# Optimization experiments

Hardware: AMD Instinct MI355X
Metric: run time of the kernel (lower is better)

The kernel has to match this reference:

```python
import jax, jax.numpy as jnp
import numpy as np

N, K, C = 128, 64, 64

def _w(key, shape, scale):
    return (jax.random.normal(key, shape, dtype=jnp.float32) * scale)

def setup_inputs() -> dict:
    key = jax.random.key(0)
    ks = jax.random.split(key, 20)
    s1 = 1.0 / np.sqrt(C)
    s2 = 1.0 / np.sqrt(2 * C)
    inp = {
        "x": jax.random.normal(ks[0], (N, K, C), dtype=jnp.float32),
        "W_lin": _w(ks[1], (C, C), s1), "b_lin": jnp.zeros((C,), jnp.float32),
        # unary_passing: Linear(C,C) -> tanh -> Linear(C,C)
        "Wu1": _w(ks[2], (C, C), s1), "bu1": jnp.zeros((C,), jnp.float32),
        "Wu2": _w(ks[3], (C, C), s1), "bu2": jnp.zeros((C,), jnp.float32),
        # unary_gate: Linear(C,C) -> tanh -> Linear(C,C) -> sigmoid
        "Wug1": _w(ks[4], (C, C), s1), "bug1": jnp.zeros((C,), jnp.float32),
        "Wug2": _w(ks[5], (C, C), s1), "bug2": jnp.zeros((C,), jnp.float32),
        # binary_passing: Linear(2C,C) -> tanh -> Linear(C,C)
        "Wb1": _w(ks[6], (2 * C, C), s2), "bb1": jnp.zeros((C,), jnp.float32),
        "Wb2": _w(ks[7], (C, C), s1), "bb2": jnp.zeros((C,), jnp.float32),
        # binary_gate: Linear(2C,C) -> tanh -> Linear(C,C) -> sigmoid
        "Wbg1": _w(ks[8], (2 * C, C), s2), "bbg1": jnp.zeros((C,), jnp.float32),
        "Wbg2": _w(ks[9], (C, C), s1), "bbg2": jnp.zeros((C,), jnp.float32),
        "t": 0,  # time scalar, ignored by IgnoreLinear base layer
    }
    return inp


def reference(x, W_lin, b_lin, Wu1, bu1, Wu2, bu2, Wug1, bug1, Wug2, bug2,
              Wb1, bb1, Wb2, bb2, Wbg1, bbg1, Wbg2, bbg2, t):
    # base linear map (IgnoreLinear: ignores t)
    h = x @ W_lin + b_lin                          # (N, K, C)
    n, k, c = h.shape
    # unary message with gate
    um = jnp.tanh(h @ Wu1 + bu1) @ Wu2 + bu2
    ug = jax.nn.sigmoid(jnp.tanh(h @ Wug1 + bug1) @ Wug2 + bug2)
    um = um * ug                                   # (N, K, C)
    # all-pairs broadcast-concat: hm[n,i,j] = [h[n,j], h[n,i]]
    hm = jnp.concatenate([
        jnp.broadcast_to(h[:, None, :, :], (n, k, k, c)),
        jnp.broadcast_to(h[:, :, None, :], (n, k, k, c)),
    ], axis=3)                                     # (N, K, K, 2C)
    bm = jnp.tanh(hm @ Wb1 + bb1) @ Wb2 + bb2      # (N, K, K, C)
    bg = jax.nn.sigmoid(jnp.tanh(hm @ Wbg1 + bbg1) @ Wbg2 + bbg2)
    # sum over axis 1 (includes diagonal, as in original), normalize by K-1
    bm = jnp.sum(bm * bg, axis=1) / jnp.float32(k - 1)  # (N, K, C)
    return um + bm
```

## Files before the change

### kernel.cpp

```cpp
#include <hip/hip_runtime.h>

#define WST 72

typedef __attribute__((ext_vector_type(4))) float    f32x4;
typedef __attribute__((ext_vector_type(2))) float    f32x2;
typedef __attribute__((ext_vector_type(8))) _Float16 f16x8;
typedef __attribute__((ext_vector_type(2))) _Float16 f16x2;

__device__ __forceinline__ float rcp_f(float x) { return __builtin_amdgcn_rcpf(x); }
__device__ __forceinline__ float fast_sigmoid(float x) {
    return rcp_f(1.0f + __expf(-x));
}
__device__ __forceinline__ float tanh_exp(float x) {
    return 1.0f - 2.0f * rcp_f(__expf(2.0f * x) + 1.0f);
}

__device__ __forceinline__ void stage512(const float* __restrict__ W,
                                         _Float16* Wt, int tid) {
#pragma unroll
    for (int i = 0; i < 8; ++i) {
        int idx = tid + i * 512;
        int k = idx >> 6, c = idx & 63;
        Wt[c * WST + k] = (_Float16)W[idx];
    }
}

__device__ __forceinline__ void gemm2(const _Float16* Act, int arow, int qd,
                                      const _Float16* Wt, int colb,
                                      f32x4 acc[2]) {
    f16x8 a0 = *(const f16x8*)(Act + arow * WST + qd * 8);
    f16x8 a1 = *(const f16x8*)(Act + arow * WST + 32 + qd * 8);
#pragma unroll
    for (int cc = 0; cc < 2; ++cc) {
        const _Float16* wr = Wt + (colb + cc * 16) * WST + qd * 8;
        f16x8 b0 = *(const f16x8*)(wr);
        f16x8 b1 = *(const f16x8*)(wr + 32);
        acc[cc] = __builtin_amdgcn_mfma_f32_16x16x32_f16(a0, b0, acc[cc], 0, 0, 0);
        acc[cc] = __builtin_amdgcn_mfma_f32_16x16x32_f16(a1, b1, acc[cc], 0, 0, 0);
    }
}

__global__ __launch_bounds__(512, 2) void fused_all_kernel(
    const float* __restrict__ x,
    const float* __restrict__ W_lin, const float* __restrict__ b_lin,
    const float* __restrict__ Wu1,  const float* __restrict__ bu1,
    const float* __restrict__ Wu2,  const float* __restrict__ bu2,
    const float* __restrict__ Wug1, const float* __restrict__ bug1,
    const float* __restrict__ Wug2, const float* __restrict__ bug2,
    const float* __restrict__ Wb1,  const float* __restrict__ bb1,
    const float* __restrict__ Wb2,  const float* __restrict__ bb2,
    const float* __restrict__ Wbg1, const float* __restrict__ bbg1,
    const float* __restrict__ Wbg2, const float* __restrict__ bbg2,
    float* __restrict__ out)
{
    __shared__ __align__(16) char smem[113664];
    _Float16* Wt0  = (_Float16*)(smem);
    _Float16* Wt1  = (_Float16*)(smem + 9216);
    _Float16* Ax   = (_Float16*)(smem + 18432);
    _Float16* Ah   = (_Float16*)(smem + 27648);
    _Float16* Au   = (_Float16*)(smem + 36864);
    _Float16* Agg  = (_Float16*)(smem + 46080);
    float*    EQb  = (float*)(smem + 55296);
    float*    EQgb = (float*)(smem + 71680);
    float*    EPm  = (float*)(smem + 88064);
    float*    EPgm = (float*)(smem + 96768);
    float*    um32 = (float*)(smem + 105472);
    float*    Red  = (float*)(smem);

    int tid = threadIdx.x, w = tid >> 6, l = tid & 63;
    int qd = l >> 4, l16 = l & 15;
    int n = blockIdx.x >> 1, jsel = blockIdx.x & 1;

    int rw = w & 3, ch = w >> 2;
    int arow = rw * 16 + l16;
    int colb = ch * 32 + l16;
    int crow = rw * 16 + qd * 4;
    bool mine = (rw >> 1) == jsel;
    int lr0 = (rw & 1) * 16 + qd * 4;

    f32x4 acc[2];

#pragma unroll
    for (int i = 0; i < 4; ++i) {
        int e = tid * 2 + i * 1024;
        f32x2 v = *(const f32x2*)(x + (size_t)n * 4096 + e);
        f16x2 p; p[0] = (_Float16)v[0]; p[1] = (_Float16)v[1];
        *(f16x2*)(Ax + (e >> 6) * WST + (e & 63)) = p;
    }
    stage512(W_lin, Wt0, tid);
    __syncthreads();

#pragma unroll
    for (int cc = 0; cc < 2; ++cc) {
        float bv = b_lin[colb + cc * 16];
        acc[cc] = (f32x4){bv, bv, bv, bv};
    }
    gemm2(Ax, arow, qd, Wt0, colb, acc);
#pragma unroll
    for (int cc = 0; cc < 2; ++cc)
#pragma unroll
        for (int r = 0; r < 4; ++r)
            Ah[(crow + r) * WST + colb + cc * 16] = (_Float16)acc[cc][r];
    stage512(Wb1, Wt1, tid);
    __syncthreads();

#pragma unroll
    for (int cc = 0; cc < 2; ++cc) {
        float bv = bb1[colb + cc * 16];
        acc[cc] = (f32x4){bv, bv, bv, bv};
    }
    gemm2(Ah, arow, qd, Wt1, colb, acc);
    if (mine) {
#pragma unroll
        for (int cc = 0; cc < 2; ++cc)
#pragma unroll
            for (int r = 0; r < 4; ++r)
                EPm[(lr0 + r) * 68 + colb + cc * 16] = __expf(2.0f * acc[cc][r]);
    }
    stage512(Wb1 + 4096, Wt0, tid);
    __syncthreads();

    acc[0] = (f32x4){0.f, 0.f, 0.f, 0.f};
    acc[1] = (f32x4){0.f, 0.f, 0.f, 0.f};
    gemm2(Ah, arow, qd, Wt0, colb, acc);
#pragma unroll
    for (int cc = 0; cc < 2; ++cc)
#pragma unroll
        for (int r = 0; r < 4; ++r)
            EQb[(crow + r) * 64 + colb + cc * 16] = __expf(2.0f * acc[cc][r]);
    stage512(Wbg1, Wt1, tid);
    __syncthreads();

#pragma unroll
    for (int cc = 0; cc < 2; ++cc) {
        float bv = bbg1[colb + cc * 16];
        acc[cc] = (f32x4){bv, bv, bv, bv};
    }
    gemm2(Ah, arow, qd, Wt1, colb, acc);
    if (mine) {
#pragma unroll
        for (int cc = 0; cc < 2; ++cc)
#pragma unroll
            for (int r = 0; r < 4; ++r)
                EPgm[(lr0 + r) * 68 + colb + cc * 16] = __expf(2.0f * acc[cc][r]);
    }
    stage512(Wbg1 + 4096, Wt0, tid);
    __syncthreads();

    acc[0] = (f32x4){0.f, 0.f, 0.f, 0.f};
    acc[1] = (f32x4){0.f, 0.f, 0.f, 0.f};
    gemm2(Ah, arow, qd, Wt0, colb, acc);
#pragma unroll
    for (int cc = 0; cc < 2; ++cc)
#pragma unroll
        for (int r = 0; r < 4; ++r)
            EQgb[(crow + r) * 64 + colb + cc * 16] = __expf(2.0f * acc[cc][r]);
    stage512(Wu1, Wt1, tid);
    __syncthreads();

#pragma unroll
    for (int cc = 0; cc < 2; ++cc) {
        float bv = bu1[colb + cc * 16];
        acc[cc] = (f32x4){bv, bv, bv, bv};
    }
    gemm2(Ah, arow, qd, Wt1, colb, acc);
#pragma unroll
    for (int cc = 0; cc < 2; ++cc)
#pragma unroll
        for (int r = 0; r < 4; ++r)
            Au[(crow + r) * WST + colb + cc * 16] = (_Float16)tanh_exp(acc[cc][r]);
    stage512(Wug1, Wt0, tid);
    __syncthreads();

#pragma unroll
    for (int cc = 0; cc < 2; ++cc) {
        float bv = bug1[colb + cc * 16];
        acc[cc] = (f32x4){bv, bv, bv, bv};
    }
    gemm2(Ah, arow, qd, Wt0, colb, acc);
#pragma unroll
    for (int cc = 0; cc < 2; ++cc)
#pragma unroll
        for (int r = 0; r < 4; ++r)
            Agg[(crow + r) * WST + colb + cc * 16] = (_Float16)tanh_exp(acc[cc][r]);
    stage512(Wu2, Wt1, tid);
    __syncthreads();

    f32x4 uacc[2];
#pragma unroll
    for (int cc = 0; cc < 2; ++cc) {
        float bv = bu2[colb + cc * 16];
        uacc[cc] = (f32x4){bv, bv, bv, bv};
    }
    gemm2(Au, arow, qd, Wt1, colb, uacc);
    stage512(Wug2, Wt0, tid);
    __syncthreads();

#pragma unroll
    for (int cc = 0; cc < 2; ++cc) {
        float bv = bug2[colb + cc * 16];
        acc[cc] = (f32x4){bv, bv, bv, bv};
    }
    gemm2(Agg, arow, qd, Wt0, colb, acc);
    if (mine) {
#pragma unroll
        for (int cc = 0; cc < 2; ++cc)
#pragma unroll
            for (int r = 0; r < 4; ++r)
                um32[(lr0 + r) * 64 + colb + cc * 16] =
                    uacc[cc][r] * fast_sigmoid(acc[cc][r]);
    }
    stage512(Wb2, Wt1, tid);
    stage512(Wbg2, Au, tid);
    __syncthreads();

    int jgrp = w >> 2, iw = w & 3;

    f16x8 bwm[4][2], bwg[4][2];
#pragma unroll
    for (int cc = 0; cc < 4; ++cc)
#pragma unroll
        for (int kk = 0; kk < 2; ++kk) {
            bwm[cc][kk] = *(const f16x8*)(Wt1 + (cc * 16 + l16) * WST + kk * 32 + qd * 8);
            bwg[cc][kk] = *(const f16x8*)(Au  + (cc * 16 + l16) * WST + kk * 32 + qd * 8);
        }
    float bim[4], big[4];
#pragma unroll
    for (int cc = 0; cc < 4; ++cc) {
        bim[cc] = bb2[cc * 16 + l16];
        big[cc] = bbg2[cc * 16 + l16];
    }

    const float* pr  = EPm  + (jgrp * 16 + l16) * 68;
    const float* pgr = EPgm + (jgrp * 16 + l16) * 68;
    f32x4 pm[4], pg[4];
    pm[0] = *(const f32x4*)(pr + qd * 8);
    pm[1] = *(const f32x4*)(pr + qd * 8 + 4);
    pm[2] = *(const f32x4*)(pr + 32 + qd * 8);
    pm[3] = *(const f32x4*)(pr + 32 + qd * 8 + 4);
    pg[0] = *(const f32x4*)(pgr + qd * 8);
    pg[1] = *(const f32x4*)(pgr + qd * 8 + 4);
    pg[2] = *(const f32x4*)(pgr + 32 + qd * 8);
    pg[3] = *(const f32x4*)(pgr + 32 + qd * 8 + 4);

    f32x4 bacc[4];
#pragma unroll
    for (int cc = 0; cc < 4; ++cc) bacc[cc] = (f32x4){0.f, 0.f, 0.f, 0.f};

    for (int ii = iw * 16; ii < iw * 16 + 16; ++ii) {
        const float* qm = EQb  + ii * 64;
        const float* qg = EQgb + ii * 64;
        f16x8 am[2], ag[2];
#pragma unroll
        for (int kk = 0; kk < 2; ++kk) {
            int cb = kk * 32 + qd * 8;
            f32x4 qa = *(const f32x4*)(qm + cb);
            f32x4 qb = *(const f32x4*)(qm + cb + 4);
            f32x4 ha = *(const f32x4*)(qg + cb);
            f32x4 hb = *(const f32x4*)(qg + cb + 4);
#pragma unroll
            for (int t = 0; t < 4; ++t) {
                am[kk][t]     = (_Float16)(1.0f - 2.0f * rcp_f(__builtin_fmaf(pm[kk*2][t],   qa[t], 1.0f)));
                am[kk][t + 4] = (_Float16)(1.0f - 2.0f * rcp_f(__builtin_fmaf(pm[kk*2+1][t], qb[t], 1.0f)));
                ag[kk][t]     = (_Float16)(1.0f - 2.0f * rcp_f(__builtin_fmaf(pg[kk*2][t],   ha[t], 1.0f)));
                ag[kk][t + 4] = (_Float16)(1.0f - 2.0f * rcp_f(__builtin_fmaf(pg[kk*2+1][t], hb[t], 1.0f)));
            }
        }
#pragma unroll
        for (int cc = 0; cc < 4; ++cc) {
            f32x4 d = {bim[cc], bim[cc], bim[cc], bim[cc]};
            d = __builtin_amdgcn_mfma_f32_16x16x32_f16(am[0], bwm[cc][0], d, 0, 0, 0);
            d = __builtin_amdgcn_mfma_f32_16x16x32_f16(am[1], bwm[cc][1], d, 0, 0, 0);
            f32x4 e = {big[cc], big[cc], big[cc], big[cc]};
            e = __builtin_amdgcn_mfma_f32_16x16x32_f16(ag[0], bwg[cc][0], e, 0, 0, 0);
            e = __builtin_amdgcn_mfma_f32_16x16x32_f16(ag[1], bwg[cc][1], e, 0, 0, 0);
#pragma unroll
            for (int r = 0; r < 4; ++r)
                bacc[cc][r] += d[r] * fast_sigmoid(e[r]);
        }
    }

    __syncthreads();
#pragma unroll
    for (int cc = 0; cc < 4; ++cc)
#pragma unroll
        for (int r = 0; r < 4; ++r)
            Red[(jgrp * 4 + iw) * 1024 + (qd * 4 + r) * 64 + cc * 16 + l16] = bacc[cc][r];
    __syncthreads();

    {
        int e = tid * 4;
        int lr = e >> 6, col = e & 63;
        int g = lr >> 4, rr = lr & 15;
        f32x4 s = {0.f, 0.f, 0.f, 0.f};
#pragma unroll
        for (int w2 = 0; w2 < 4; ++w2)
            s += *(const f32x4*)(Red + (g * 4 + w2) * 1024 + rr * 64 + col);
        f32x4 u = *(const f32x4*)(um32 + lr * 64 + col);
        f32x4 o;
#pragma unroll
        for (int t = 0; t < 4; ++t)
            o[t] = u[t] + s[t] * (1.0f / 63.0f);
        *(f32x4*)(out + (size_t)n * 4096 + (size_t)(jsel * 32 + lr) * 64 + col) = o;
    }
}

extern "C" void kernel_launch(void* const* d_in, const int* in_sizes, int n_in,
                              void* d_out, int out_size, void* d_ws, size_t ws_size,
                              hipStream_t stream)
{
    (void)in_sizes; (void)n_in; (void)out_size; (void)d_ws; (void)ws_size;
    const float* x     = (const float*)d_in[0];
    const float* W_lin = (const float*)d_in[1];
    const float* b_lin = (const float*)d_in[2];
    const float* Wu1   = (const float*)d_in[3];
    const float* bu1   = (const float*)d_in[4];
    const float* Wu2   = (const float*)d_in[5];
    const float* bu2   = (const float*)d_in[6];
    const float* Wug1  = (const float*)d_in[7];
    const float* bug1  = (const float*)d_in[8];
    const float* Wug2  = (const float*)d_in[9];
    const float* bug2  = (const float*)d_in[10];
    const float* Wb1   = (const float*)d_in[11];
    const float* bb1   = (const float*)d_in[12];
    const float* Wb2   = (const float*)d_in[13];
    const float* bb2   = (const float*)d_in[14];
    const float* Wbg1  = (const float*)d_in[15];
    const float* bbg1  = (const float*)d_in[16];
    const float* Wbg2  = (const float*)d_in[17];
    const float* bbg2  = (const float*)d_in[18];

    hipLaunchKernelGGL(fused_all_kernel, dim3(256), dim3(512), 0, stream,
        x, W_lin, b_lin, Wu1, bu1, Wu2, bu2, Wug1, bug1, Wug2, bug2,
        Wb1, bb1, Wb2, bb2, Wbg1, bbg1, Wbg2, bbg2,
        (float*)d_out);
}
```

Baseline: 118.7 us.

## Double block size, restructure prologue staging, and fold tanh/sigmoid algebra into weights

Launches 1024-thread blocks instead of 512, splitting the prologue GEMMs so each wave computes one 16-column tile and restaging weights into registers ahead of use to overlap global loads with compute. The tanh affine part is folded into pre-scaled second-layer weights and column-sum biases, the sigmoid uses exp2 with a pre-multiplied log2e, and pairs of reciprocals share one rcp via a product trick with packed fp16 conversion. The main pair loop runs 8 rows per wave across 16 waves, and the reduction sums 8 partials. This trades the previous two-blocks-per-CU occupancy for one larger block, and the shared reciprocals risk overflow or precision loss.

Result: slower. 194.1 us (+63.6%).

```diff
diff --git a/kernel.cpp b/kernel.cpp
--- a/kernel.cpp
+++ b/kernel.cpp
@@ -1,46 +1,55 @@
 #include <hip/hip_runtime.h>
 
 #define WST 72
+#define LOG2E 1.44269504f
 
 typedef __attribute__((ext_vector_type(4))) float    f32x4;
 typedef __attribute__((ext_vector_type(2))) float    f32x2;
 typedef __attribute__((ext_vector_type(8))) _Float16 f16x8;
+typedef __attribute__((ext_vector_type(4))) _Float16 f16x4;
 typedef __attribute__((ext_vector_type(2))) _Float16 f16x2;
+typedef __attribute__((ext_vector_type(2))) __fp16   fp16x2_raw;
+
+union U8 { f16x8 v; f16x2 h[4]; };
 
 __device__ __forceinline__ float rcp_f(float x) { return __builtin_amdgcn_rcpf(x); }
+__device__ __forceinline__ float exp2_f(float x) { return __builtin_amdgcn_exp2f(x); }
 __device__ __forceinline__ float fast_sigmoid(float x) {
     return rcp_f(1.0f + __expf(-x));
 }
 __device__ __forceinline__ float tanh_exp(float x) {
     return 1.0f - 2.0f * rcp_f(__expf(2.0f * x) + 1.0f);
 }
-
-__device__ __forceinline__ void stage512(const float* __restrict__ W,
-                                         _Float16* Wt, int tid) {
-#pragma unroll
-    for (int i = 0; i < 8; ++i) {
-        int idx = tid + i * 512;
-        int k = idx >> 6, c = idx & 63;
-        Wt[c * WST + k] = (_Float16)W[idx];
-    }
-}
-
-__device__ __forceinline__ void gemm2(const _Float16* Act, int arow, int qd,
-                                      const _Float16* Wt, int colb,
-                                      f32x4 acc[2]) {
+__device__ __forceinline__ f16x2 pkrtz(float a, float b) {
+    fp16x2_raw r = __builtin_amdgcn_cvt_pkrtz(a, b);
+    return __builtin_bit_cast(f16x2, r);
+}
+
+__device__ __forceinline__ void wload4(const float* __restrict__ W, int tid, float v[4]) {
+#pragma unroll
+    for (int i = 0; i < 4; ++i) v[i] = W[tid + i * 1024];
+}
+__device__ __forceinline__ void wstore4(_Float16* Wt, int tid, const float v[4], float scale) {
+#pragma unroll
+    for (int i = 0; i < 4; ++i) {
+        int idx = tid + i * 1024;
+        Wt[(idx & 63) * WST + (idx >> 6)] = (_Float16)(v[i] * scale);
+    }
+}
+
+__device__ __forceinline__ f32x4 gemm1(const _Float16* Act, int arow, int qd,
+                                       const _Float16* Wt, int bcol, f32x4 acc) {
     f16x8 a0 = *(const f16x8*)(Act + arow * WST + qd * 8);
     f16x8 a1 = *(const f16x8*)(Act + arow * WST + 32 + qd * 8);
-#pragma unroll
-    for (int cc = 0; cc < 2; ++cc) {
-        const _Float16* wr = Wt + (colb + cc * 16) * WST + qd * 8;
-        f16x8 b0 = *(const f16x8*)(wr);
-        f16x8 b1 = *(const f16x8*)(wr + 32);
-        acc[cc] = __builtin_amdgcn_mfma_f32_16x16x32_f16(a0, b0, acc[cc], 0, 0, 0);
-        acc[cc] = __builtin_amdgcn_mfma_f32_16x16x32_f16(a1, b1, acc[cc], 0, 0, 0);
-    }
-}
-
-__global__ __launch_bounds__(512, 2) void fused_all_kernel(
+    const _Float16* wr = Wt + bcol * WST + qd * 8;
+    f16x8 b0 = *(const f16x8*)(wr);
+    f16x8 b1 = *(const f16x8*)(wr + 32);
+    acc = __builtin_amdgcn_mfma_f32_16x16x32_f16(a0, b0, acc, 0, 0, 0);
+    acc = __builtin_amdgcn_mfma_f32_16x16x32_f16(a1, b1, acc, 0, 0, 0);
+    return acc;
+}
+
+__global__ __launch_bounds__(1024) void fused_all_kernel(
     const float* __restrict__ x,
     const float* __restrict__ W_lin, const float* __restrict__ b_lin,
     const float* __restrict__ Wu1,  const float* __restrict__ bu1,
@@ -53,182 +62,181 @@
     const float* __restrict__ Wbg2, const float* __restrict__ bbg2,
     float* __restrict__ out)
 {
-    __shared__ __align__(16) char smem[113664];
-    _Float16* Wt0  = (_Float16*)(smem);
-    _Float16* Wt1  = (_Float16*)(smem + 9216);
-    _Float16* Ax   = (_Float16*)(smem + 18432);
-    _Float16* Ah   = (_Float16*)(smem + 27648);
-    _Float16* Au   = (_Float16*)(smem + 36864);
-    _Float16* Agg  = (_Float16*)(smem + 46080);
-    float*    EQb  = (float*)(smem + 55296);
-    float*    EQgb = (float*)(smem + 71680);
-    float*    EPm  = (float*)(smem + 88064);
-    float*    EPgm = (float*)(smem + 96768);
+    __shared__ __align__(16) char smem[114176];
+    _Float16* S0 = (_Float16*)(smem);
+    _Float16* S1 = (_Float16*)(smem + 9216);
+    _Float16* S2 = (_Float16*)(smem + 18432);
+    _Float16* S3 = (_Float16*)(smem + 27648);
+    _Float16* S4 = (_Float16*)(smem + 36864);
+    _Float16* S5 = (_Float16*)(smem + 46080);
+    float*    EPm  = (float*)(smem + 55296);
+    float*    EPgm = (float*)(smem + 64000);
+    float*    EQb  = (float*)(smem + 72704);
+    float*    EQgb = (float*)(smem + 89088);
     float*    um32 = (float*)(smem + 105472);
+    float*    csum_m = (float*)(smem + 113664);
+    float*    csum_g = (float*)(smem + 113920);
     float*    Red  = (float*)(smem);
 
     int tid = threadIdx.x, w = tid >> 6, l = tid & 63;
     int qd = l >> 4, l16 = l & 15;
     int n = blockIdx.x >> 1, jsel = blockIdx.x & 1;
 
-    int rw = w & 3, ch = w >> 2;
-    int arow = rw * 16 + l16;
-    int colb = ch * 32 + l16;
-    int crow = rw * 16 + qd * 4;
-    bool mine = (rw >> 1) == jsel;
-    int lr0 = (rw & 1) * 16 + qd * 4;
-
-    f32x4 acc[2];
-
-#pragma unroll
-    for (int i = 0; i < 4; ++i) {
-        int e = tid * 2 + i * 1024;
-        f32x2 v = *(const f32x2*)(x + (size_t)n * 4096 + e);
-        f16x2 p; p[0] = (_Float16)v[0]; p[1] = (_Float16)v[1];
-        *(f16x2*)(Ax + (e >> 6) * WST + (e & 63)) = p;
-    }
-    stage512(W_lin, Wt0, tid);
-    __syncthreads();
-
-#pragma unroll
-    for (int cc = 0; cc < 2; ++cc) {
-        float bv = b_lin[colb + cc * 16];
-        acc[cc] = (f32x4){bv, bv, bv, bv};
-    }
-    gemm2(Ax, arow, qd, Wt0, colb, acc);
-#pragma unroll
-    for (int cc = 0; cc < 2; ++cc)
-#pragma unroll
-        for (int r = 0; r < 4; ++r)
-            Ah[(crow + r) * WST + colb + cc * 16] = (_Float16)acc[cc][r];
-    stage512(Wb1, Wt1, tid);
-    __syncthreads();
-
-#pragma unroll
-    for (int cc = 0; cc < 2; ++cc) {
-        float bv = bb1[colb + cc * 16];
-        acc[cc] = (f32x4){bv, bv, bv, bv};
-    }
-    gemm2(Ah, arow, qd, Wt1, colb, acc);
-    if (mine) {
-#pragma unroll
-        for (int cc = 0; cc < 2; ++cc)
-#pragma unroll
-            for (int r = 0; r < 4; ++r)
-                EPm[(lr0 + r) * 68 + colb + cc * 16] = __expf(2.0f * acc[cc][r]);
-    }
-    stage512(Wb1 + 4096, Wt0, tid);
-    __syncthreads();
-
-    acc[0] = (f32x4){0.f, 0.f, 0.f, 0.f};
-    acc[1] = (f32x4){0.f, 0.f, 0.f, 0.f};
-    gemm2(Ah, arow, qd, Wt0, colb, acc);
-#pragma unroll
-    for (int cc = 0; cc < 2; ++cc)
-#pragma unroll
-        for (int r = 0; r < 4; ++r)
-            EQb[(crow + r) * 64 + colb + cc * 16] = __expf(2.0f * acc[cc][r]);
-    stage512(Wbg1, Wt1, tid);
-    __syncthreads();
-
-#pragma unroll
-    for (int cc = 0; cc < 2; ++cc) {
-        float bv = bbg1[colb + cc * 16];
-        acc[cc] = (f32x4){bv, bv, bv, bv};
-    }
-    gemm2(Ah, arow, qd, Wt1, colb, acc);
-    if (mine) {
-#pragma unroll
-        for (int cc = 0; cc < 2; ++cc)
-#pragma unroll
-            for (int r = 0; r < 4; ++r)
-                EPgm[(lr0 + r) * 68 + colb + cc * 16] = __expf(2.0f * acc[cc][r]);
-    }
-    stage512(Wbg1 + 4096, Wt0, tid);
-    __syncthreads();
-
-    acc[0] = (f32x4){0.f, 0.f, 0.f, 0.f};
-    acc[1] = (f32x4){0.f, 0.f, 0.f, 0.f};
-    gemm2(Ah, arow, qd, Wt0, colb, acc);
-#pragma unroll
-    for (int cc = 0; cc < 2; ++cc)
-#pragma unroll
-        for (int r = 0; r < 4; ++r)
-            EQgb[(crow + r) * 64 + colb + cc * 16] = __expf(2.0f * acc[cc][r]);
-    stage512(Wu1, Wt1, tid);
-    __syncthreads();
-
-#pragma unroll
-    for (int cc = 0; cc < 2; ++cc) {
-        float bv = bu1[colb + cc * 16];
-        acc[cc] = (f32x4){bv, bv, bv, bv};
-    }
-    gemm2(Ah, arow, qd, Wt1, colb, acc);
-#pragma unroll
-    for (int cc = 0; cc < 2; ++cc)
-#pragma unroll
-        for (int r = 0; r < 4; ++r)
-            Au[(crow + r) * WST + colb + cc * 16] = (_Float16)tanh_exp(acc[cc][r]);
-    stage512(Wug1, Wt0, tid);
-    __syncthreads();
-
-#pragma unroll
-    for (int cc = 0; cc < 2; ++cc) {
-        float bv = bug1[colb + cc * 16];
-        acc[cc] = (f32x4){bv, bv, bv, bv};
-    }
-    gemm2(Ah, arow, qd, Wt0, colb, acc);
-#pragma unroll
-    for (int cc = 0; cc < 2; ++cc)
-#pragma unroll
-        for (int r = 0; r < 4; ++r)
-            Agg[(crow + r) * WST + colb + cc * 16] = (_Float16)tanh_exp(acc[cc][r]);
-    stage512(Wu2, Wt1, tid);
-    __syncthreads();
-
-    f32x4 uacc[2];
-#pragma unroll
-    for (int cc = 0; cc < 2; ++cc) {
-        float bv = bu2[colb + cc * 16];
-        uacc[cc] = (f32x4){bv, bv, bv, bv};
-    }
-    gemm2(Au, arow, qd, Wt1, colb, uacc);
-    stage512(Wug2, Wt0, tid);
-    __syncthreads();
-
-#pragma unroll
-    for (int cc = 0; cc < 2; ++cc) {
-        float bv = bug2[colb + cc * 16];
-        acc[cc] = (f32x4){bv, bv, bv, bv};
-    }
-    gemm2(Agg, arow, qd, Wt0, colb, acc);
-    if (mine) {
-#pragma unroll
-        for (int cc = 0; cc < 2; ++cc)
-#pragma unroll
-            for (int r = 0; r < 4; ++r)
-                um32[(lr0 + r) * 64 + colb + cc * 16] =
-                    uacc[cc][r] * fast_sigmoid(acc[cc][r]);
-    }
-    stage512(Wb2, Wt1, tid);
-    stage512(Wbg2, Au, tid);
-    __syncthreads();
-
-    int jgrp = w >> 2, iw = w & 3;
+    int rw = w & 3, cw = w >> 2;
+    int arow64 = rw * 16 + l16;
+    int bcol64 = cw * 16 + l16;
+    int crow64 = rw * 16 + qd * 4;
+
+    int w8 = w & 7;
+    int rw2 = w8 & 1, cw2 = w8 >> 1;
+    int lrow32 = rw2 * 16;
+    int bcol32 = cw2 * 16 + l16;
+    bool loW = (w < 8);
+
+    {
+        float wv[4];
+        wload4(W_lin, tid, wv);
+        int e = tid * 4;
+        f32x4 v = *(const f32x4*)(x + (size_t)n * 4096 + e);
+        f16x4 p;
+#pragma unroll
+        for (int t = 0; t < 4; ++t) p[t] = (_Float16)v[t];
+        *(f16x4*)(S2 + (e >> 6) * WST + (e & 63)) = p;
+        wstore4(S0, tid, wv, 1.0f);
+    }
+    __syncthreads();
+
+    {
+        float wa[4], wb[4];
+        wload4(Wb1, tid, wa);
+        wload4(Wb1 + 4096, tid, wb);
+        float bv = b_lin[bcol64];
+        f32x4 acc = (f32x4){bv, bv, bv, bv};
+        acc = gemm1(S2, arow64, qd, S0, bcol64, acc);
+#pragma unroll
+        for (int r = 0; r < 4; ++r)
+            S3[(crow64 + r) * WST + bcol64] = (_Float16)acc[r];
+        wstore4(S1, tid, wa, 1.0f);
+        wstore4(S4, tid, wb, 1.0f);
+    }
+    __syncthreads();
+
+    {
+        float wa[4], wb[4];
+        wload4(Wbg1, tid, wa);
+        wload4(Wbg1 + 4096, tid, wb);
+        f32x4 acc = (f32x4){0.f, 0.f, 0.f, 0.f};
+        acc = gemm1(S3, arow64, qd, S4, bcol64, acc);
+#pragma unroll
+        for (int r = 0; r < 4; ++r)
+            EQb[(crow64 + r) * 64 + bcol64] = __expf(2.0f * acc[r]);
+        wstore4(S2, tid, wa, 1.0f);
+        wstore4(S0, tid, wb, 1.0f);
+    }
+    __syncthreads();
+
+    {
+        float wa[4], wb[4];
+        wload4(Wu1, tid, wa);
+        wload4(Wu2, tid, wb);
+        const _Float16* Bw = loW ? S1 : S2;
+        const float* b1 = loW ? bb1 : bbg1;
+        float* dst = loW ? EPm : EPgm;
+        float bv = b1[bcol32];
+        f32x4 acc = (f32x4){bv, bv, bv, bv};
+        acc = gemm1(S3, jsel * 32 + lrow32 + l16, qd, Bw, bcol32, acc);
+#pragma unroll
+        for (int r = 0; r < 4; ++r)
+            dst[(lrow32 + qd * 4 + r) * 68 + bcol32] = __expf(2.0f * acc[r]);
+        wstore4(S4, tid, wa, 1.0f);
+        wstore4(S5, tid, wb, 1.0f);
+    }
+    __syncthreads();
+
+    {
+        float wa[4], wb[4];
+        wload4(Wug1, tid, wa);
+        wload4(Wug2, tid, wb);
+        f32x4 acc = (f32x4){0.f, 0.f, 0.f, 0.f};
+        acc = gemm1(S3, arow64, qd, S0, bcol64, acc);
+#pragma unroll
+        for (int r = 0; r < 4; ++r)
+            EQgb[(crow64 + r) * 64 + bcol64] = __expf(2.0f * acc[r]);
+        wstore4(S1, tid, wa, 1.0f);
+        wstore4(S2, tid, wb, 1.0f);
+    }
+    __syncthreads();
+
+    {
+        const _Float16* Bw = loW ? S4 : S1;
+        const float* b1 = loW ? bu1 : bug1;
+        _Float16* Tdst = loW ? S0 : (S0 + 2304);
+        float bv = b1[bcol32];
+        f32x4 acc = (f32x4){bv, bv, bv, bv};
+        acc = gemm1(S3, jsel * 32 + lrow32 + l16, qd, Bw, bcol32, acc);
+#pragma unroll
+        for (int r = 0; r < 4; ++r)
+            Tdst[(lrow32 + qd * 4 + r) * WST + bcol32] = (_Float16)tanh_exp(acc[r]);
+    }
+    __syncthreads();
+
+    if (loW) {
+        float bv = bu2[bcol32];
+        f32x4 ua = (f32x4){bv, bv, bv, bv};
+        ua = gemm1(S0, lrow32 + l16, qd, S5, bcol32, ua);
+        bv = bug2[bcol32];
+        f32x4 ga = (f32x4){bv, bv, bv, bv};
+        ga = gemm1(S0 + 2304, lrow32 + l16, qd, S2, bcol32, ga);
+#pragma unroll
+        for (int r = 0; r < 4; ++r)
+            um32[(lrow32 + qd * 4 + r) * 64 + bcol32] = ua[r] * fast_sigmoid(ga[r]);
+    } else {
+        int tid2 = tid - 512;
+        float wm[8], wg[8];
+#pragma unroll
+        for (int i = 0; i < 8; ++i) {
+            wm[i] = Wb2[tid2 + i * 512];
+            wg[i] = Wbg2[tid2 + i * 512];
+        }
+        if (w == 8) {
+            float cs = 0.0f;
+#pragma unroll 16
+            for (int k = 0; k < 64; ++k)
+                cs += (float)(_Float16)(-2.0f * Wb2[k * 64 + l]);
+            csum_m[l] = bb2[l] - 0.5f * cs;
+        }
+        if (w == 9) {
+            float cs = 0.0f;
+#pragma unroll 16
+            for (int k = 0; k < 64; ++k)
+                cs += (float)(_Float16)(2.0f * LOG2E * Wbg2[k * 64 + l]);
+            csum_g[l] = -LOG2E * bbg2[l] - 0.5f * cs;
+        }
+#pragma unroll
+        for (int i = 0; i < 8; ++i) {
+            int idx = tid2 + i * 512;
+            int o = (idx & 63) * WST + (idx >> 6);
+            S1[o] = (_Float16)(wm[i] * -2.0f);
+            S3[o] = (_Float16)(wg[i] * (2.0f * LOG2E));
+        }
+    }
+    __syncthreads();
+
+    int jgrp = w >> 3, iw = w & 7;
 
     f16x8 bwm[4][2], bwg[4][2];
 #pragma unroll
     for (int cc = 0; cc < 4; ++cc)
 #pragma unroll
         for (int kk = 0; kk < 2; ++kk) {
-            bwm[cc][kk] = *(const f16x8*)(Wt1 + (cc * 16 + l16) * WST + kk * 32 + qd * 8);
-            bwg[cc][kk] = *(const f16x8*)(Au  + (cc * 16 + l16) * WST + kk * 32 + qd * 8);
+            bwm[cc][kk] = *(const f16x8*)(S1 + (cc * 16 + l16) * WST + kk * 32 + qd * 8);
+            bwg[cc][kk] = *(const f16x8*)(S3 + (cc * 16 + l16) * WST + kk * 32 + qd * 8);
         }
     float bim[4], big[4];
 #pragma unroll
     for (int cc = 0; cc < 4; ++cc) {
-        bim[cc] = bb2[cc * 16 + l16];
-        big[cc] = bbg2[cc * 16 + l16];
+        bim[cc] = csum_m[cc * 16 + l16];
+        big[cc] = csum_g[cc * 16 + l16];
     }
 
     const float* pr  = EPm  + (jgrp * 16 + l16) * 68;
@@ -247,10 +255,10 @@
 #pragma unroll
     for (int cc = 0; cc < 4; ++cc) bacc[cc] = (f32x4){0.f, 0.f, 0.f, 0.f};
 
-    for (int ii = iw * 16; ii < iw * 16 + 16; ++ii) {
+    for (int ii = iw * 8; ii < iw * 8 + 8; ++ii) {
         const float* qm = EQb  + ii * 64;
         const float* qg = EQgb + ii * 64;
-        f16x8 am[2], ag[2];
+        U8 am[2], ag[2];
 #pragma unroll
         for (int kk = 0; kk < 2; ++kk) {
             int cb = kk * 32 + qd * 8;
@@ -259,24 +267,43 @@
             f32x4 ha = *(const f32x4*)(qg + cb);
             f32x4 hb = *(const f32x4*)(qg + cb + 4);
 #pragma unroll
-            for (int t = 0; t < 4; ++t) {
-                am[kk][t]     = (_Float16)(1.0f - 2.0f * rcp_f(__builtin_fmaf(pm[kk*2][t],   qa[t], 1.0f)));
-                am[kk][t + 4] = (_Float16)(1.0f - 2.0f * rcp_f(__builtin_fmaf(pm[kk*2+1][t], qb[t], 1.0f)));
-                ag[kk][t]     = (_Float16)(1.0f - 2.0f * rcp_f(__builtin_fmaf(pg[kk*2][t],   ha[t], 1.0f)));
-                ag[kk][t + 4] = (_Float16)(1.0f - 2.0f * rcp_f(__builtin_fmaf(pg[kk*2+1][t], hb[t], 1.0f)));
+            for (int t = 0; t < 2; ++t) {
+                float a0 = __builtin_fmaf(pm[kk*2][2*t],   qa[2*t],   1.0f);
+                float a1 = __builtin_fmaf(pm[kk*2][2*t+1], qa[2*t+1], 1.0f);
+                float ri = rcp_f(a0 * a1);
+                am[kk].h[t]     = pkrtz(ri * a1, ri * a0);
+                float b0f = __builtin_fmaf(pm[kk*2+1][2*t],   qb[2*t],   1.0f);
+                float b1f = __builtin_fmaf(pm[kk*2+1][2*t+1], qb[2*t+1], 1.0f);
+                float rj = rcp_f(b0f * b1f);
+                am[kk].h[2 + t] = pkrtz(rj * b1f, rj * b0f);
+                float c0 = __builtin_fmaf(pg[kk*2][2*t],   ha[2*t],   1.0f);
+                float c1 = __builtin_fmaf(pg[kk*2][2*t+1], ha[2*t+1], 1.0f);
+                float rk = rcp_f(c0 * c1);
+                ag[kk].h[t]     = pkrtz(rk * c1, rk * c0);
+                float d0 = __builtin_fmaf(pg[kk*2+1][2*t],   hb[2*t],   1.0f);
+                float d1 = __builtin_fmaf(pg[kk*2+1][2*t+1], hb[2*t+1], 1.0f);
+                float rl = rcp_f(d0 * d1);
+                ag[kk].h[2 + t] = pkrtz(rl * d1, rl * d0);
             }
         }
 #pragma unroll
         for (int cc = 0; cc < 4; ++cc) {
             f32x4 d = {bim[cc], bim[cc], bim[cc], bim[cc]};
-            d = __builtin_amdgcn_mfma_f32_16x16x32_f16(am[0], bwm[cc][0], d, 0, 0, 0);
-            d = __builtin_amdgcn_mfma_f32_16x16x32_f16(am[1], bwm[cc][1], d, 0, 0, 0);
+            d = __builtin_amdgcn_mfma_f32_16x16x32_f16(am[0].v, bwm[cc][0], d, 0, 0, 0);
+            d = __builtin_amdgcn_mfma_f32_16x16x32_f16(am[1].v, bwm[cc][1], d, 0, 0, 0);
             f32x4 e = {big[cc], big[cc], big[cc], big[cc]};
-            e = __builtin_amdgcn_mfma_f32_16x16x32_f16(ag[0], bwg[cc][0], e, 0, 0, 0);
-            e = __builtin_amdgcn_mfma_f32_16x16x32_f16(ag[1], bwg[cc][1], e, 0, 0, 0);
-#pragma unroll
-            for (int r = 0; r < 4; ++r)
-                bacc[cc][r] += d[r] * fast_sigmoid(e[r]);
+            e = __builtin_amdgcn_mfma_f32_16x16x32_f16(ag[0].v, bwg[cc][0], e, 0, 0, 0);
+            e = __builtin_amdgcn_mfma_f32_16x16x32_f16(ag[1].v, bwg[cc][1], e, 0, 0, 0);
+            float v0 = exp2_f(e[0]), v1 = exp2_f(e[1]);
+            float u0 = 1.0f + v0, u1 = 1.0f + v1;
+            float r01 = rcp_f(u0 * u1);
+            bacc[cc][0] = __builtin_fmaf(d[0] * u1, r01, bacc[cc][0]);
+            bacc[cc][1] = __builtin_fmaf(d[1] * u0, r01, bacc[cc][1]);
+            float v2 = exp2_f(e[2]), v3 = exp2_f(e[3]);
+            float u2 = 1.0f + v2, u3 = 1.0f + v3;
+            float r23 = rcp_f(u2 * u3);
+            bacc[cc][2] = __builtin_fmaf(d[2] * u3, r23, bacc[cc][2]);
+            bacc[cc][3] = __builtin_fmaf(d[3] * u2, r23, bacc[cc][3]);
         }
     }
 
@@ -285,23 +312,22 @@
     for (int cc = 0; cc < 4; ++cc)
 #pragma unroll
         for (int r = 0; r < 4; ++r)
-            Red[(jgrp * 4 + iw) * 1024 + (qd * 4 + r) * 64 + cc * 16 + l16] = bacc[cc][r];
-    __syncthreads();
-
-    {
-        int e = tid * 4;
+            Red[(jgrp * 8 + iw) * 1024 + (qd * 4 + r) * 64 + cc * 16 + l16] = bacc[cc][r];
+    __syncthreads();
+
+    {
+        int e = tid * 2;
         int lr = e >> 6, col = e & 63;
         int g = lr >> 4, rr = lr & 15;
-        f32x4 s = {0.f, 0.f, 0.f, 0.f};
-#pragma unroll
-        for (int w2 = 0; w2 < 4; ++w2)
-            s += *(const f32x4*)(Red + (g * 4 + w2) * 1024 + rr * 64 + col);
-        f32x4 u = *(const f32x4*)(um32 + lr * 64 + col);
-        f32x4 o;
-#pragma unroll
-        for (int t = 0; t < 4; ++t)
-            o[t] = u[t] + s[t] * (1.0f / 63.0f);
-        *(f32x4*)(out + (size_t)n * 4096 + (size_t)(jsel * 32 + lr) * 64 + col) = o;
+        f32x2 s = {0.f, 0.f};
+#pragma unroll
+        for (int p = 0; p < 8; ++p)
+            s += *(const f32x2*)(Red + (g * 8 + p) * 1024 + rr * 64 + col);
+        f32x2 u = *(const f32x2*)(um32 + lr * 64 + col);
+        f32x2 o;
+        o[0] = u[0] + s[0] * (1.0f / 63.0f);
+        o[1] = u[1] + s[1] * (1.0f / 63.0f);
+        *(f32x2*)(out + (size_t)n * 4096 + (size_t)(jsel * 32 + lr) * 64 + col) = o;
     }
 }
 
@@ -330,7 +356,7 @@
     const float* Wbg2  = (const float*)d_in[17];
     const float* bbg2  = (const float*)d_in[18];
 
-    hipLaunchKernelGGL(fused_all_kernel, dim3(256), dim3(512), 0, stream,
+    hipLaunchKernelGGL(fused_all_kernel, dim3(256), dim3(1024), 0, stream,
         x, W_lin, b_lin, Wu1, bu1, Wu2, bu2, Wug1, bug1, Wug2, bug2,
         Wb1, bb1, Wb2, bb2, Wbg1, bbg1, Wbg2, bbg2,
         (float*)d_out);
```

## Batch weight staging, split prologue GEMMs by wave, fold tanh/sigmoid constants into weights

Applied to the files above, without the earlier changes.

Weight staging now prefetches several matrices into registers and writes them alongside the GEMM work, so the prologue needs far fewer barriers. The unary and pair GEMMs are split so each wave group only computes the 32 rows that this block needs. In the all-pairs loop, the tanh affine constants (1 - 2r) and the sigmoid log2e scaling are folded into pre-scaled Wb2/Wbg2 and adjusted biases via column sums. This leaves raw reciprocals, exp2, paired reciprocals sharing one rcp, and packed RTZ conversions. It raises shared memory to about 149 KB, which likely keeps occupancy at one block per CU, and adds small precision risk from fp16 scaled weights, rounding-toward-zero conversion and products in the shared reciprocals.

New measurement: 117.4 us. Within noise of the previous version (-1.1%).

```diff
diff --git a/kernel.cpp b/kernel.cpp
--- a/kernel.cpp
+++ b/kernel.cpp
@@ -1,28 +1,43 @@
 #include <hip/hip_runtime.h>
 
 #define WST 72
+#define LOG2E 1.44269504f
 
 typedef __attribute__((ext_vector_type(4))) float    f32x4;
 typedef __attribute__((ext_vector_type(2))) float    f32x2;
 typedef __attribute__((ext_vector_type(8))) _Float16 f16x8;
 typedef __attribute__((ext_vector_type(2))) _Float16 f16x2;
+typedef __attribute__((ext_vector_type(2))) __fp16   fp16x2_raw;
+
+union U8 { f16x8 v; f16x2 h[4]; };
 
 __device__ __forceinline__ float rcp_f(float x) { return __builtin_amdgcn_rcpf(x); }
+__device__ __forceinline__ float exp2_f(float x) { return __builtin_amdgcn_exp2f(x); }
 __device__ __forceinline__ float fast_sigmoid(float x) {
     return rcp_f(1.0f + __expf(-x));
 }
 __device__ __forceinline__ float tanh_exp(float x) {
     return 1.0f - 2.0f * rcp_f(__expf(2.0f * x) + 1.0f);
 }
-
-__device__ __forceinline__ void stage512(const float* __restrict__ W,
-                                         _Float16* Wt, int tid) {
+__device__ __forceinline__ f16x2 pkrtz(float a, float b) {
+    fp16x2_raw r = __builtin_amdgcn_cvt_pkrtz(a, b);
+    return __builtin_bit_cast(f16x2, r);
+}
+
+__device__ __forceinline__ void wload8(const float* __restrict__ W, int tid, float v[8]) {
+#pragma unroll
+    for (int i = 0; i < 8; ++i) v[i] = W[tid + i * 512];
+}
+__device__ __forceinline__ void wstore8(_Float16* Wt, int tid, const float v[8], float scale) {
 #pragma unroll
     for (int i = 0; i < 8; ++i) {
         int idx = tid + i * 512;
-        int k = idx >> 6, c = idx & 63;
-        Wt[c * WST + k] = (_Float16)W[idx];
-    }
+        Wt[(idx & 63) * WST + (idx >> 6)] = (_Float16)(v[i] * scale);
+    }
+}
+__device__ __forceinline__ void wload16(const float* __restrict__ W, int t256, float v[16]) {
+#pragma unroll
+    for (int i = 0; i < 16; ++i) v[i] = W[t256 + i * 256];
 }
 
 __device__ __forceinline__ void gemm2(const _Float16* Act, int arow, int qd,
@@ -53,18 +68,23 @@
     const float* __restrict__ Wbg2, const float* __restrict__ bbg2,
     float* __restrict__ out)
 {
-    __shared__ __align__(16) char smem[113664];
-    _Float16* Wt0  = (_Float16*)(smem);
-    _Float16* Wt1  = (_Float16*)(smem + 9216);
-    _Float16* Ax   = (_Float16*)(smem + 18432);
-    _Float16* Ah   = (_Float16*)(smem + 27648);
-    _Float16* Au   = (_Float16*)(smem + 36864);
-    _Float16* Agg  = (_Float16*)(smem + 46080);
-    float*    EQb  = (float*)(smem + 55296);
-    float*    EQgb = (float*)(smem + 71680);
-    float*    EPm  = (float*)(smem + 88064);
-    float*    EPgm = (float*)(smem + 96768);
-    float*    um32 = (float*)(smem + 105472);
+    __shared__ __align__(16) char smem[152576];
+    _Float16* WLs = (_Float16*)(smem);
+    _Float16* SX  = (_Float16*)(smem + 9216);
+    _Float16* SH  = (_Float16*)(smem + 18432);
+    _Float16* W1  = (_Float16*)(smem + 27648);
+    _Float16* W2  = (_Float16*)(smem + 36864);
+    _Float16* W3  = (_Float16*)(smem + 46080);
+    _Float16* W4  = (_Float16*)(smem + 55296);
+    _Float16* W5  = (_Float16*)(smem + 64512);
+    _Float16* W6  = (_Float16*)(smem + 73728);
+    _Float16* W7  = (_Float16*)(smem + 82944);
+    float*    EPm  = (float*)(smem + 92160);
+    float*    EPgm = (float*)(smem + 100864);
+    float*    EQb  = (float*)(smem + 109568);
+    float*    EQgb = (float*)(smem + 125952);
+    float*    um32 = (float*)(smem + 142336);
+    float*    csP  = (float*)(smem + 150528);
     float*    Red  = (float*)(smem);
 
     int tid = threadIdx.x, w = tid >> 6, l = tid & 63;
@@ -75,8 +95,11 @@
     int arow = rw * 16 + l16;
     int colb = ch * 32 + l16;
     int crow = rw * 16 + qd * 4;
-    bool mine = (rw >> 1) == jsel;
-    int lr0 = (rw & 1) * 16 + qd * 4;
+
+    int s = w & 3;
+    int lr16 = (s & 1) * 16;
+    int cb32 = (s >> 1) * 32;
+    bool loW = (w < 4);
 
     f32x4 acc[2];
 
@@ -85,133 +108,148 @@
         int e = tid * 2 + i * 1024;
         f32x2 v = *(const f32x2*)(x + (size_t)n * 4096 + e);
         f16x2 p; p[0] = (_Float16)v[0]; p[1] = (_Float16)v[1];
-        *(f16x2*)(Ax + (e >> 6) * WST + (e & 63)) = p;
-    }
-    stage512(W_lin, Wt0, tid);
-    __syncthreads();
-
-#pragma unroll
-    for (int cc = 0; cc < 2; ++cc) {
-        float bv = b_lin[colb + cc * 16];
-        acc[cc] = (f32x4){bv, bv, bv, bv};
-    }
-    gemm2(Ax, arow, qd, Wt0, colb, acc);
-#pragma unroll
-    for (int cc = 0; cc < 2; ++cc)
-#pragma unroll
-        for (int r = 0; r < 4; ++r)
-            Ah[(crow + r) * WST + colb + cc * 16] = (_Float16)acc[cc][r];
-    stage512(Wb1, Wt1, tid);
-    __syncthreads();
-
-#pragma unroll
-    for (int cc = 0; cc < 2; ++cc) {
-        float bv = bb1[colb + cc * 16];
-        acc[cc] = (f32x4){bv, bv, bv, bv};
-    }
-    gemm2(Ah, arow, qd, Wt1, colb, acc);
-    if (mine) {
-#pragma unroll
-        for (int cc = 0; cc < 2; ++cc)
-#pragma unroll
-            for (int r = 0; r < 4; ++r)
-                EPm[(lr0 + r) * 68 + colb + cc * 16] = __expf(2.0f * acc[cc][r]);
-    }
-    stage512(Wb1 + 4096, Wt0, tid);
-    __syncthreads();
-
-    acc[0] = (f32x4){0.f, 0.f, 0.f, 0.f};
-    acc[1] = (f32x4){0.f, 0.f, 0.f, 0.f};
-    gemm2(Ah, arow, qd, Wt0, colb, acc);
-#pragma unroll
-    for (int cc = 0; cc < 2; ++cc)
-#pragma unroll
-        for (int r = 0; r < 4; ++r)
-            EQb[(crow + r) * 64 + colb + cc * 16] = __expf(2.0f * acc[cc][r]);
-    stage512(Wbg1, Wt1, tid);
-    __syncthreads();
-
-#pragma unroll
-    for (int cc = 0; cc < 2; ++cc) {
-        float bv = bbg1[colb + cc * 16];
-        acc[cc] = (f32x4){bv, bv, bv, bv};
-    }
-    gemm2(Ah, arow, qd, Wt1, colb, acc);
-    if (mine) {
-#pragma unroll
-        for (int cc = 0; cc < 2; ++cc)
-#pragma unroll
-            for (int r = 0; r < 4; ++r)
-                EPgm[(lr0 + r) * 68 + colb + cc * 16] = __expf(2.0f * acc[cc][r]);
-    }
-    stage512(Wbg1 + 4096, Wt0, tid);
-    __syncthreads();
-
-    acc[0] = (f32x4){0.f, 0.f, 0.f, 0.f};
-    acc[1] = (f32x4){0.f, 0.f, 0.f, 0.f};
-    gemm2(Ah, arow, qd, Wt0, colb, acc);
-#pragma unroll
-    for (int cc = 0; cc < 2; ++cc)
-#pragma unroll
-        for (int r = 0; r < 4; ++r)
-            EQgb[(crow + r) * 64 + colb + cc * 16] = __expf(2.0f * acc[cc][r]);
-    stage512(Wu1, Wt1, tid);
-    __syncthreads();
-
-#pragma unroll
-    for (int cc = 0; cc < 2; ++cc) {
-        float bv = bu1[colb + cc * 16];
-        acc[cc] = (f32x4){bv, bv, bv, bv};
-    }
-    gemm2(Ah, arow, qd, Wt1, colb, acc);
-#pragma unroll
-    for (int cc = 0; cc < 2; ++cc)
-#pragma unroll
-        for (int r = 0; r < 4; ++r)
-            Au[(crow + r) * WST + colb + cc * 16] = (_Float16)tanh_exp(acc[cc][r]);
-    stage512(Wug1, Wt0, tid);
-    __syncthreads();
-
-#pragma unroll
-    for (int cc = 0; cc < 2; ++cc) {
-        float bv = bug1[colb + cc * 16];
-        acc[cc] = (f32x4){bv, bv, bv, bv};
-    }
-    gemm2(Ah, arow, qd, Wt0, colb, acc);
-#pragma unroll
-    for (int cc = 0; cc < 2; ++cc)
-#pragma unroll
-        for (int r = 0; r < 4; ++r)
-            Agg[(crow + r) * WST + colb + cc * 16] = (_Float16)tanh_exp(acc[cc][r]);
-    stage512(Wu2, Wt1, tid);
-    __syncthreads();
-
-    f32x4 uacc[2];
-#pragma unroll
-    for (int cc = 0; cc < 2; ++cc) {
-        float bv = bu2[colb + cc * 16];
-        uacc[cc] = (f32x4){bv, bv, bv, bv};
-    }
-    gemm2(Au, arow, qd, Wt1, colb, uacc);
-    stage512(Wug2, Wt0, tid);
-    __syncthreads();
-
-#pragma unroll
-    for (int cc = 0; cc < 2; ++cc) {
-        float bv = bug2[colb + cc * 16];
-        acc[cc] = (f32x4){bv, bv, bv, bv};
-    }
-    gemm2(Agg, arow, qd, Wt0, colb, acc);
-    if (mine) {
-#pragma unroll
-        for (int cc = 0; cc < 2; ++cc)
-#pragma unroll
-            for (int r = 0; r < 4; ++r)
-                um32[(lr0 + r) * 64 + colb + cc * 16] =
-                    uacc[cc][r] * fast_sigmoid(acc[cc][r]);
-    }
-    stage512(Wb2, Wt1, tid);
-    stage512(Wbg2, Au, tid);
+        *(f16x2*)(SX + (e >> 6) * WST + (e & 63)) = p;
+    }
+    {
+        float wv[8];
+        wload8(W_lin, tid, wv);
+        wstore8(WLs, tid, wv, 1.0f);
+    }
+    __syncthreads();
+
+    {
+        float wv0[8], wv1[8], wv2[8], wv3[8], wv4[8], wv5[8];
+        wload8(Wb1, tid, wv0);
+        wload8(Wb1 + 4096, tid, wv1);
+        wload8(Wbg1, tid, wv2);
+        wload8(Wbg1 + 4096, tid, wv3);
+        wload8(Wu1, tid, wv4);
+        wload8(Wug1, tid, wv5);
+#pragma unroll
+        for (int cc = 0; cc < 2; ++cc) {
+            float bv = b_lin[colb + cc * 16];
+            acc[cc] = (f32x4){bv, bv, bv, bv};
+        }
+        gemm2(SX, arow, qd, WLs, colb, acc);
+#pragma unroll
+        for (int cc = 0; cc < 2; ++cc)
+#pragma unroll
+            for (int r = 0; r < 4; ++r)
+                SH[(crow + r) * WST + colb + cc * 16] = (_Float16)acc[cc][r];
+        wstore8(W1, tid, wv0, 1.0f);
+        wstore8(W2, tid, wv1, 1.0f);
+        wstore8(W3, tid, wv2, 1.0f);
+        wstore8(W4, tid, wv3, 1.0f);
+        wstore8(W5, tid, wv4, 1.0f);
+        wstore8(W6, tid, wv5, 1.0f);
+    }
+    __syncthreads();
+
+    {
+        float wu2v[8], wug2v[8];
+        wload8(Wu2, tid, wu2v);
+        wload8(Wug2, tid, wug2v);
+
+        acc[0] = (f32x4){0.f, 0.f, 0.f, 0.f};
+        acc[1] = (f32x4){0.f, 0.f, 0.f, 0.f};
+        gemm2(SH, arow, qd, W2, colb, acc);
+#pragma unroll
+        for (int cc = 0; cc < 2; ++cc)
+#pragma unroll
+            for (int r = 0; r < 4; ++r)
+                EQb[(crow + r) * 64 + colb + cc * 16] = __expf(2.0f * acc[cc][r]);
+
+        f32x4 accg[2];
+        accg[0] = (f32x4){0.f, 0.f, 0.f, 0.f};
+        accg[1] = (f32x4){0.f, 0.f, 0.f, 0.f};
+        gemm2(SH, arow, qd, W4, colb, accg);
+#pragma unroll
+        for (int cc = 0; cc < 2; ++cc)
+#pragma unroll
+            for (int r = 0; r < 4; ++r)
+                EQgb[(crow + r) * 64 + colb + cc * 16] = __expf(2.0f * accg[cc][r]);
+
+        const _Float16* Wp = loW ? W1 : W3;
+        const _Float16* Wt = loW ? W5 : W6;
+        const float* bp = loW ? bb1 : bbg1;
+        const float* bt = loW ? bu1 : bug1;
+        float* EPdst = loW ? EPm : EPgm;
+        _Float16* Tdst = loW ? WLs : (WLs + 2304);
+
+        f32x4 accp[2];
+#pragma unroll
+        for (int cc = 0; cc < 2; ++cc) {
+            float bv = bp[cb32 + cc * 16 + l16];
+            accp[cc] = (f32x4){bv, bv, bv, bv};
+        }
+        gemm2(SH, jsel * 32 + lr16 + l16, qd, Wp, cb32 + l16, accp);
+#pragma unroll
+        for (int cc = 0; cc < 2; ++cc)
+#pragma unroll
+            for (int r = 0; r < 4; ++r)
+                EPdst[(lr16 + qd * 4 + r) * 68 + cb32 + cc * 16 + l16] =
+                    __expf(2.0f * accp[cc][r]);
+
+        f32x4 acct[2];
+#pragma unroll
+        for (int cc = 0; cc < 2; ++cc) {
+            float bv = bt[cb32 + cc * 16 + l16];
+            acct[cc] = (f32x4){bv, bv, bv, bv};
+        }
+        gemm2(SH, jsel * 32 + lr16 + l16, qd, Wt, cb32 + l16, acct);
+#pragma unroll
+        for (int cc = 0; cc < 2; ++cc)
+#pragma unroll
+            for (int r = 0; r < 4; ++r)
+                Tdst[(lr16 + qd * 4 + r) * WST + cb32 + cc * 16 + l16] =
+                    (_Float16)tanh_exp(acct[cc][r]);
+
+        wstore8(SX, tid, wu2v, 1.0f);
+        wstore8(W7, tid, wug2v, 1.0f);
+    }
+    __syncthreads();
+
+    if (loW) {
+        f32x4 ua[2], ga[2];
+#pragma unroll
+        for (int cc = 0; cc < 2; ++cc) {
+            float bv = bu2[cb32 + cc * 16 + l16];
+            ua[cc] = (f32x4){bv, bv, bv, bv};
+        }
+        gemm2(WLs, lr16 + l16, qd, SX, cb32 + l16, ua);
+#pragma unroll
+        for (int cc = 0; cc < 2; ++cc) {
+            float bv = bug2[cb32 + cc * 16 + l16];
+            ga[cc] = (f32x4){bv, bv, bv, bv};
+        }
+        gemm2(WLs + 2304, lr16 + l16, qd, W7, cb32 + l16, ga);
+#pragma unroll
+        for (int cc = 0; cc < 2; ++cc)
+#pragma unroll
+            for (int r = 0; r < 4; ++r)
+                um32[(lr16 + qd * 4 + r) * 64 + cb32 + cc * 16 + l16] =
+                    ua[cc][r] * fast_sigmoid(ga[cc][r]);
+    } else {
+        int tid2 = tid - 256;
+        float wm[16], wg[16];
+        wload16(Wb2, tid2, wm);
+        wload16(Wbg2, tid2, wg);
+        float csm = 0.0f, csg = 0.0f;
+#pragma unroll
+        for (int i = 0; i < 16; ++i) {
+            int idx = tid2 + i * 256;
+            int o = (idx & 63) * WST + (idx >> 6);
+            _Float16 a = (_Float16)(wm[i] * -2.0f);
+            _Float16 b = (_Float16)(wg[i] * (2.0f * LOG2E));
+            W1[o] = a;
+            W2[o] = b;
+            csm += (float)a;
+            csg += (float)b;
+        }
+        int q = tid2 >> 6, c = tid2 & 63;
+        csP[q * 64 + c] = csm;
+        csP[256 + q * 64 + c] = csg;
+    }
     __syncthreads();
 
     int jgrp = w >> 2, iw = w & 3;
@@ -221,14 +259,17 @@
     for (int cc = 0; cc < 4; ++cc)
 #pragma unroll
         for (int kk = 0; kk < 2; ++kk) {
-            bwm[cc][kk] = *(const f16x8*)(Wt1 + (cc * 16 + l16) * WST + kk * 32 + qd * 8);
-            bwg[cc][kk] = *(const f16x8*)(Au  + (cc * 16 + l16) * WST + kk * 32 + qd * 8);
+            bwm[cc][kk] = *(const f16x8*)(W1 + (cc * 16 + l16) * WST + kk * 32 + qd * 8);
+            bwg[cc][kk] = *(const f16x8*)(W2 + (cc * 16 + l16) * WST + kk * 32 + qd * 8);
         }
     float bim[4], big[4];
 #pragma unroll
     for (int cc = 0; cc < 4; ++cc) {
-        bim[cc] = bb2[cc * 16 + l16];
-        big[cc] = bbg2[cc * 16 + l16];
+        int c = cc * 16 + l16;
+        bim[cc] = bb2[c] -
+            0.5f * (csP[c] + csP[64 + c] + csP[128 + c] + csP[192 + c]);
+        big[cc] = -LOG2E * bbg2[c] -
+            0.5f * (csP[256 + c] + csP[320 + c] + csP[384 + c] + csP[448 + c]);
     }
 
     const float* pr  = EPm  + (jgrp * 16 + l16) * 68;
@@ -250,7 +291,7 @@
     for (int ii = iw * 16; ii < iw * 16 + 16; ++ii) {
         const float* qm = EQb  + ii * 64;
         const float* qg = EQgb + ii * 64;
-        f16x8 am[2], ag[2];
+        U8 am[2], ag[2];
 #pragma unroll
         for (int kk = 0; kk < 2; ++kk) {
             int cb = kk * 32 + qd * 8;
@@ -259,24 +300,43 @@
             f32x4 ha = *(const f32x4*)(qg + cb);
             f32x4 hb = *(const f32x4*)(qg + cb + 4);
 #pragma unroll
-            for (int t = 0; t < 4; ++t) {
-                am[kk][t]     = (_Float16)(1.0f - 2.0f * rcp_f(__builtin_fmaf(pm[kk*2][t],   qa[t], 1.0f)));
-                am[kk][t + 4] = (_Float16)(1.0f - 2.0f * rcp_f(__builtin_fmaf(pm[kk*2+1][t], qb[t], 1.0f)));
-                ag[kk][t]     = (_Float16)(1.0f - 2.0f * rcp_f(__builtin_fmaf(pg[kk*2][t],   ha[t], 1.0f)));
-                ag[kk][t + 4] = (_Float16)(1.0f - 2.0f * rcp_f(__builtin_fmaf(pg[kk*2+1][t], hb[t], 1.0f)));
+            for (int t = 0; t < 2; ++t) {
+                float a0 = __builtin_fmaf(pm[kk*2][2*t],   qa[2*t],   1.0f);
+                float a1 = __builtin_fmaf(pm[kk*2][2*t+1], qa[2*t+1], 1.0f);
+                float ri = rcp_f(a0 * a1);
+                am[kk].h[t]     = pkrtz(ri * a1, ri * a0);
+                float b0f = __builtin_fmaf(pm[kk*2+1][2*t],   qb[2*t],   1.0f);
+                float b1f = __builtin_fmaf(pm[kk*2+1][2*t+1], qb[2*t+1], 1.0f);
+                float rj = rcp_f(b0f * b1f);
+                am[kk].h[2 + t] = pkrtz(rj * b1f, rj * b0f);
+                float c0 = __builtin_fmaf(pg[kk*2][2*t],   ha[2*t],   1.0f);
+                float c1 = __builtin_fmaf(pg[kk*2][2*t+1], ha[2*t+1], 1.0f);
+                float rk = rcp_f(c0 * c1);
+                ag[kk].h[t]     = pkrtz(rk * c1, rk * c0);
+                float d0 = __builtin_fmaf(pg[kk*2+1][2*t],   hb[2*t],   1.0f);
+                float d1 = __builtin_fmaf(pg[kk*2+1][2*t+1], hb[2*t+1], 1.0f);
+                float rl = rcp_f(d0 * d1);
+                ag[kk].h[2 + t] = pkrtz(rl * d1, rl * d0);
             }
         }
 #pragma unroll
         for (int cc = 0; cc < 4; ++cc) {
             f32x4 d = {bim[cc], bim[cc], bim[cc], bim[cc]};
-            d = __builtin_amdgcn_mfma_f32_16x16x32_f16(am[0], bwm[cc][0], d, 0, 0, 0);
-            d = __builtin_amdgcn_mfma_f32_16x16x32_f16(am[1], bwm[cc][1], d, 0, 0, 0);
+            d = __builtin_amdgcn_mfma_f32_16x16x32_f16(am[0].v, bwm[cc][0], d, 0, 0, 0);
+            d = __builtin_amdgcn_mfma_f32_16x16x32_f16(am[1].v, bwm[cc][1], d, 0, 0, 0);
             f32x4 e = {big[cc], big[cc], big[cc], big[cc]};
-            e = __builtin_amdgcn_mfma_f32_16x16x32_f16(ag[0], bwg[cc][0], e, 0, 0, 0);
-            e = __builtin_amdgcn_mfma_f32_16x16x32_f16(ag[1], bwg[cc][1], e, 0, 0, 0);
-#pragma unroll
-            for (int r = 0; r < 4; ++r)
-                bacc[cc][r] += d[r] * fast_sigmoid(e[r]);
+            e = __builtin_amdgcn_mfma_f32_16x16x32_f16(ag[0].v, bwg[cc][0], e, 0, 0, 0);
+            e = __builtin_amdgcn_mfma_f32_16x16x32_f16(ag[1].v, bwg[cc][1], e, 0, 0, 0);
+            float v0 = exp2_f(e[0]), v1 = exp2_f(e[1]);
+            float u0 = 1.0f + v0, u1 = 1.0f + v1;
+            float r01 = rcp_f(u0 * u1);
+            bacc[cc][0] = __builtin_fmaf(d[0] * u1, r01, bacc[cc][0]);
+            bacc[cc][1] = __builtin_fmaf(d[1] * u0, r01, bacc[cc][1]);
+            float v2 = exp2_f(e[2]), v3 = exp2_f(e[3]);
+            float u2 = 1.0f + v2, u3 = 1.0f + v3;
+            float r23 = rcp_f(u2 * u3);
+            bacc[cc][2] = __builtin_fmaf(d[2] * u3, r23, bacc[cc][2]);
+            bacc[cc][3] = __builtin_fmaf(d[3] * u2, r23, bacc[cc][3]);
         }
     }
 
@@ -292,15 +352,15 @@
         int e = tid * 4;
         int lr = e >> 6, col = e & 63;
         int g = lr >> 4, rr = lr & 15;
-        f32x4 s = {0.f, 0.f, 0.f, 0.f};
-#pragma unroll
-        for (int w2 = 0; w2 < 4; ++w2)
-            s += *(const f32x4*)(Red + (g * 4 + w2) * 1024 + rr * 64 + col);
+        f32x4 sv = {0.f, 0.f, 0.f, 0.f};
+#pragma unroll
+        for (int p = 0; p < 4; ++p)
+            sv += *(const f32x4*)(Red + (g * 4 + p) * 1024 + rr * 64 + col);
         f32x4 u = *(const f32x4*)(um32 + lr * 64 + col);
         f32x4 o;
 #pragma unroll
         for (int t = 0; t < 4; ++t)
-            o[t] = u[t] + s[t] * (1.0f / 63.0f);
+            o[t] = u[t] + sv[t] * (1.0f / 63.0f);
         *(f32x4*)(out + (size_t)n * 4096 + (size_t)(jsel * 32 + lr) * 64 + col) = o;
     }
 }
```
